# Kernel optimization log

Measured on AMD Instinct MI355X. Metric: run time of the kernel, lower is better.

The kernel has to match this reference:

```python
import jax, jax.numpy as jnp
import numpy as np

B, S, D, M, E, K = 2, 2048, 1024, 1408, 8, 2  # batch, seq, n_embed, n_moe_mlp, n_experts, top_k


def setup_inputs() -> dict:
    key = jax.random.key(0)
    k0, k1, k2, k3, k4 = jax.random.split(key, 5)
    scale = 0.02
    return {
        "x": jax.random.normal(k0, (B, S, D), dtype=jnp.float32),
        "w_gate": jax.random.normal(k1, (D, E), dtype=jnp.float32) * scale,  # gate.weight.T
        "w_g": jax.random.normal(k2, (E, D, M), dtype=jnp.float32) * scale,  # gate_proj.weight.T per expert
        "w_u": jax.random.normal(k3, (E, D, M), dtype=jnp.float32) * scale,  # up_proj.weight.T per expert
        "w_d": jax.random.normal(k4, (E, M, D), dtype=jnp.float32) * scale,  # down_proj.weight.T per expert
    }


def reference(x, w_gate, w_g, w_u, w_d):
    # router
    scores = x @ w_gate                                  # [B,S,E]
    topk_scores, topk_idx = jax.lax.top_k(scores, K)     # [B,S,K]
    topk_probs = jax.nn.softmax(topk_scores, axis=-1)    # softmax over selected experts only
    # scatter top-k probs back to dense [B,S,E] gating (top_k indices are distinct)
    gating = jnp.sum(
        jax.nn.one_hot(topk_idx, E, dtype=topk_probs.dtype) * topk_probs[..., None],
        axis=-2,
    )                                                    # [B,S,E]
    # dense all-expert SwiGLU (faithful to the compute-then-mask original)
    hidden = jax.nn.silu(jnp.einsum("bsd,edm->ebsm", x, w_g)) * jnp.einsum(
        "bsd,edm->ebsm", x, w_u
    )                                                    # [E,B,S,M]
    expert_out = jnp.einsum("ebsm,emd->ebsd", hidden, w_d)  # [E,B,S,D]
    # masked weighted combine
    y = jnp.einsum("bse,ebsd->bsd", gating, expert_out)  # [B,S,D]
    return y
```

## Files before the change

kernel.cpp:

```cpp
#include <hip/hip_runtime.h>
#include <cstdio>

constexpr int T  = 4096;
constexpr int D  = 1024;
constexpr int M  = 1408;
constexpr int E  = 8;

constexpr int TM = 128;
constexpr int TN = 128;
constexpr int BK = 32;
constexpr int MT_MAX = T / TM;
constexpr int NT_UP = M / TN;
constexpr int NT_DN = D / TN;
constexpr int RCAP = T * 2 + E * TM;

constexpr int CSTR = 64;
constexpr int XCV  = T / 2;
constexpr int TPW  = E * (D / 64) * (M / 64);
constexpr int PREP_GRID = XCV + 2 * TPW;
constexpr int NGEMM_UP  = E * MT_MAX * NT_UP;
constexpr int UPG_GRID  = NGEMM_UP + TPW;

typedef _Float16 half8 __attribute__((ext_vector_type(8)));
typedef float    floatx4 __attribute__((ext_vector_type(4)));

#define VMW12() asm volatile("s_waitcnt vmcnt(12)" ::: "memory")
#define VMW6()  asm volatile("s_waitcnt vmcnt(6)"  ::: "memory")
#define VMW4()  asm volatile("s_waitcnt vmcnt(4)"  ::: "memory")
#define VMW0()  asm volatile("s_waitcnt vmcnt(0)"  ::: "memory")

constexpr size_t OFF_COUNTS = 0;
constexpr size_t OFF_TLIST  = 2048;
constexpr size_t OFF_PLIST  = OFF_TLIST + (size_t)E * T * 4;
constexpr size_t OFF_XH     = OFF_PLIST + (size_t)E * T * 4;
constexpr size_t OFF_HID    = OFF_XH  + (size_t)T * D * 2;
constexpr size_t OFF_WGT    = OFF_HID + (size_t)RCAP * M * 2;
constexpr size_t OFF_WUT    = OFF_WGT + (size_t)E * M * D * 2;
constexpr size_t OFF_WDT    = OFF_WUT + (size_t)E * M * D * 2;
constexpr size_t WS_NEED    = OFF_WDT + (size_t)E * D * M * 2;

__device__ __forceinline__ void gl_lds16(const void* g, void* l) {
  __builtin_amdgcn_global_load_lds(
      (const __attribute__((address_space(1))) unsigned int*)g,
      (__attribute__((address_space(3))) unsigned int*)l, 16, 0, 0);
}

__device__ __forceinline__ void expert_base_pc(const int* __restrict__ counts,
                                               int e, int& base_e, int& pc_e,
                                               int& cnt_e) {
  int b = 0; base_e = 0; pc_e = 0; cnt_e = 0;
  #pragma unroll
  for (int ee = 0; ee < E; ++ee) {
    int c = counts[ee * CSTR];
    int p = (c + TM - 1) / TM * TM;
    if (ee == e) { base_e = b; pc_e = p; cnt_e = c; }
    b += p;
  }
}

__device__ __forceinline__ void transpose64(
    const float* __restrict__ src, _Float16* __restrict__ dst,
    int Rr, int Cc, int j, float (*tile)[69]) {
  int ctn = Cc >> 6, rtn = Rr >> 6;
  int e   = j / (ctn * rtn);
  int rem = j - e * (ctn * rtn);
  int rt = rem / ctn, ct = rem - rt * ctn;
  int t = threadIdx.x;
  int lr = t >> 2;
  int lc = (t & 3) * 16;
  const float* s = src + ((size_t)e * Rr + rt * 64 + lr) * Cc + ct * 64 + lc;
  float4 v0 = *(const float4*)(s + 0);
  float4 v1 = *(const float4*)(s + 4);
  float4 v2 = *(const float4*)(s + 8);
  float4 v3 = *(const float4*)(s + 12);
  float* tr = &tile[lr][lc];
  tr[0]  = v0.x; tr[1]  = v0.y; tr[2]  = v0.z; tr[3]  = v0.w;
  tr[4]  = v1.x; tr[5]  = v1.y; tr[6]  = v1.z; tr[7]  = v1.w;
  tr[8]  = v2.x; tr[9]  = v2.y; tr[10] = v2.z; tr[11] = v2.w;
  tr[12] = v3.x; tr[13] = v3.y; tr[14] = v3.z; tr[15] = v3.w;
  __syncthreads();
  #pragma unroll
  for (int rep = 0; rep < 2; ++rep) {
    int s2 = t + rep * 256;
    int oc = s2 >> 3;
    int sl = s2 & 7;
    half8 o;
    #pragma unroll
    for (int q = 0; q < 8; ++q) o[q] = (_Float16)tile[sl * 8 + q][oc];
    *(half8*)(dst + ((size_t)e * Cc + ct * 64 + oc) * Rr + rt * 64 + sl * 8) = o;
  }
}

__global__ __launch_bounds__(256) void k_prep(
    const float* __restrict__ x, const float* __restrict__ wgate,
    const float* __restrict__ w_g, const float* __restrict__ w_u,
    _Float16* __restrict__ Xh,
    _Float16* __restrict__ wgT, _Float16* __restrict__ wuT,
    int* __restrict__ counts, int* __restrict__ tlist,
    float* __restrict__ plist) {
  __shared__ float tile[64][69];
  __shared__ float s_red[4][8];
  int bid = blockIdx.x;

  if (bid < XCV) {
    int tid = threadIdx.x;
    int row  = tid >> 7;
    int t    = bid * 2 + row;
    int dpos = (tid & 127) * 8;
    int wv = tid >> 6, lane = tid & 63;
    const float* xr = x + (size_t)t * D + dpos;
    float4 v0 = *(const float4*)(xr);
    float4 v1 = *(const float4*)(xr + 4);
    half8 h;
    h[0] = (_Float16)v0.x; h[1] = (_Float16)v0.y;
    h[2] = (_Float16)v0.z; h[3] = (_Float16)v0.w;
    h[4] = (_Float16)v1.x; h[5] = (_Float16)v1.y;
    h[6] = (_Float16)v1.z; h[7] = (_Float16)v1.w;
    *(half8*)(Xh + (size_t)t * D + dpos) = h;
    float xv[8] = {v0.x, v0.y, v0.z, v0.w, v1.x, v1.y, v1.z, v1.w};
    float acc[8] = {0.f,0.f,0.f,0.f,0.f,0.f,0.f,0.f};
    #pragma unroll
    for (int j = 0; j < 8; ++j) {
      const float4* wr2 = (const float4*)(wgate + (size_t)(dpos + j) * E);
      float4 w0 = wr2[0], w1 = wr2[1];
      acc[0] += xv[j] * w0.x; acc[1] += xv[j] * w0.y;
      acc[2] += xv[j] * w0.z; acc[3] += xv[j] * w0.w;
      acc[4] += xv[j] * w1.x; acc[5] += xv[j] * w1.y;
      acc[6] += xv[j] * w1.z; acc[7] += xv[j] * w1.w;
    }
    #pragma unroll
    for (int e = 0; e < 8; ++e) {
      #pragma unroll
      for (int off = 32; off; off >>= 1) acc[e] += __shfl_xor(acc[e], off, 64);
    }
    if (lane == 0) {
      #pragma unroll
      for (int e = 0; e < 8; ++e) s_red[wv][e] = acc[e];
    }
    __syncthreads();
    if ((tid & 127) == 0) {
      int wb = row * 2;
      float sc[8];
      #pragma unroll
      for (int e = 0; e < 8; ++e) sc[e] = s_red[wb][e] + s_red[wb + 1][e];
      int i0 = 0; float s0 = sc[0];
      #pragma unroll
      for (int e = 1; e < 8; ++e) if (sc[e] > s0) { s0 = sc[e]; i0 = e; }
      int i1 = -1; float s1 = -1e30f;
      #pragma unroll
      for (int e = 0; e < 8; ++e) if (e != i0 && sc[e] > s1) { s1 = sc[e]; i1 = e; }
      float p0 = 1.f / (1.f + expf(s1 - s0));
      float p1 = 1.f - p0;
      int q0 = atomicAdd(&counts[i0 * CSTR], 1);
      int q1 = atomicAdd(&counts[i1 * CSTR], 1);
      tlist[i0 * T + q0] = t; plist[i0 * T + q0] = p0;
      tlist[i1 * T + q1] = t; plist[i1 * T + q1] = p1;
    }
    return;
  }

  int i = bid - XCV;
  if (i < TPW) transpose64(w_g, wgT, D, M, i, tile);
  else         transpose64(w_u, wuT, D, M, i - TPW, tile);
}

__global__ __launch_bounds__(256, 2) void k_upgate(
    const _Float16* __restrict__ Xh, const _Float16* __restrict__ wgT,
    const _Float16* __restrict__ wuT, _Float16* __restrict__ Hid,
    const int* __restrict__ counts, const int* __restrict__ tlist,
    const float* __restrict__ w_d, _Float16* __restrict__ wdT) {
  __shared__ _Float16 As[3][TM * BK];
  __shared__ _Float16 Bg[3][TN * BK];
  __shared__ _Float16 Bu[3][TN * BK];
  int lin = blockIdx.x;
  if (lin >= NGEMM_UP) {
    float (*tile)[69] = reinterpret_cast<float (*)[69]>(&As[0][0]);
    transpose64(w_d, wdT, M, D, lin - NGEMM_UP, tile);
    return;
  }
  int e = lin & 7;
  int r = lin >> 3;
  int nt = r % NT_UP;
  int mt = r / NT_UP;
  int base_e, pc_e, cnt_e;
  expert_base_pc(counts, e, base_e, pc_e, cnt_e);
  if (mt * TM >= pc_e) return;
  int row0 = base_e + mt * TM;
  int n0 = nt * TN;
  int tid = threadIdx.x;
  int w = tid >> 6, lane = tid & 63;
  int lrow = lane & 15, quad = lane >> 4;
  int wr = w >> 1, wc = w & 1;
  int sr = lane >> 2;
  int c4 = lane & 3;
  int swc = ((c4 ^ ((sr >> 1) & 3))) * 8;

  const _Float16* wg_e = wgT + (size_t)e * M * D;
  const _Float16* wu_e = wuT + (size_t)e * M * D;
  const _Float16* pA[2]; const _Float16* pG[2]; const _Float16* pU[2];
  int loff[2];
  #pragma unroll
  for (int is = 0; is < 2; ++is) {
    int grow = w * 32 + is * 16 + sr;
    int local = mt * TM + grow;
    int trow = (local < cnt_e) ? tlist[e * T + local] : 0;
    pA[is] = Xh   + (size_t)trow * D + swc;
    pG[is] = wg_e + (size_t)(n0 + grow) * D + swc;
    pU[is] = wu_e + (size_t)(n0 + grow) * D + swc;
    loff[is] = (w * 2 + is) * 1024;
  }

  int swr = (lrow >> 1) & 3;

  floatx4 accg[4][4] = {};
  floatx4 accu[4][4] = {};

  auto stage = [&](int b) {
    char* a0 = (char*)&As[b][0];
    char* g0 = (char*)&Bg[b][0];
    char* u0 = (char*)&Bu[b][0];
    #pragma unroll
    for (int is = 0; is < 2; ++is) {
      gl_lds16(pA[is], a0 + loff[is]); pA[is] += BK;
      gl_lds16(pG[is], g0 + loff[is]); pG[is] += BK;
      gl_lds16(pU[is], u0 + loff[is]); pU[is] += BK;
    }
  };
  auto compute = [&](int b) {
    int kc = (quad ^ swr) * 8;
    half8 af[4];
    #pragma unroll
    for (int i = 0; i < 4; ++i)
      af[i] = *(const half8*)&As[b][(wr * 64 + i * 16 + lrow) * BK + kc];
    #pragma unroll
    for (int c = 0; c < 4; ++c) {
      int bo = (wc * 64 + c * 16 + lrow) * BK + kc;
      half8 bgc = *(const half8*)&Bg[b][bo];
      half8 buc = *(const half8*)&Bu[b][bo];
      #pragma unroll
      for (int i = 0; i < 4; ++i) {
        accg[c][i] = __builtin_amdgcn_mfma_f32_16x16x32_f16(af[i], bgc, accg[c][i], 0, 0, 0);
        accu[c][i] = __builtin_amdgcn_mfma_f32_16x16x32_f16(af[i], buc, accu[c][i], 0, 0, 0);
      }
    }
  };

  constexpr int NTK = D / BK;
  stage(0); stage(1);
  for (int k = 0; k < NTK; ++k) {
    if (k + 2 < NTK) {
      stage((k + 2) % 3);
      VMW12();
    } else if (k + 1 < NTK) {
      VMW6();
    } else {
      VMW0();
    }
    __builtin_amdgcn_sched_barrier(0);
    __builtin_amdgcn_s_barrier();
    compute(k % 3);
    __builtin_amdgcn_s_barrier();
  }

  #pragma unroll
  for (int c = 0; c < 4; ++c) {
    int col = n0 + wc * 64 + c * 16 + lrow;
    #pragma unroll
    for (int i = 0; i < 4; ++i) {
      int rowb = row0 + wr * 64 + i * 16 + quad * 4;
      #pragma unroll
      for (int reg = 0; reg < 4; ++reg) {
        float g = accg[c][i][reg], u = accu[c][i][reg];
        Hid[(size_t)(rowb + reg) * M + col] = (_Float16)(g / (1.f + expf(-g)) * u);
      }
    }
  }
}

__global__ __launch_bounds__(256, 2) void k_down(
    const _Float16* __restrict__ Hid, const _Float16* __restrict__ wdT,
    float* __restrict__ out, const int* __restrict__ counts,
    const int* __restrict__ tlist, const float* __restrict__ plist) {
  int lin = blockIdx.x;
  int e = lin & 7;
  int r = lin >> 3;
  int nt = r % NT_DN;
  int mt = r / NT_DN;
  int base_e, pc_e, cnt_e;
  expert_base_pc(counts, e, base_e, pc_e, cnt_e);
  if (mt * TM >= pc_e) return;
  int row0 = base_e + mt * TM;
  int d0 = nt * TN;
  __shared__ _Float16 As[2][TM * BK];
  __shared__ _Float16 Bs[2][TN * BK];
  int tid = threadIdx.x;
  int w = tid >> 6, lane = tid & 63;
  int lrow = lane & 15, quad = lane >> 4;
  int wr = w >> 1, wc = w & 1;
  int sr = lane >> 2;
  int c4 = lane & 3;
  int swc = ((c4 ^ ((sr >> 1) & 3))) * 8;

  const _Float16* wd_e = wdT + (size_t)e * D * M;
  const _Float16* pA[2]; const _Float16* pB[2];
  int loff[2];
  #pragma unroll
  for (int is = 0; is < 2; ++is) {
    int grow = w * 32 + is * 16 + sr;
    pA[is] = Hid  + (size_t)(row0 + grow) * M + swc;
    pB[is] = wd_e + (size_t)(d0   + grow) * M + swc;
    loff[is] = (w * 2 + is) * 1024;
  }

  int swr = (lrow >> 1) & 3;

  floatx4 acc[4][4] = {};

  auto stage = [&](int b) {
    char* a0 = (char*)&As[b][0];
    char* b0 = (char*)&Bs[b][0];
    #pragma unroll
    for (int is = 0; is < 2; ++is) {
      gl_lds16(pA[is], a0 + loff[is]); pA[is] += BK;
      gl_lds16(pB[is], b0 + loff[is]); pB[is] += BK;
    }
  };
  auto compute = [&](int b) {
    int kc = (quad ^ swr) * 8;
    half8 af[4];
    #pragma unroll
    for (int i = 0; i < 4; ++i)
      af[i] = *(const half8*)&As[b][(wr * 64 + i * 16 + lrow) * BK + kc];
    #pragma unroll
    for (int c = 0; c < 4; ++c) {
      half8 bc = *(const half8*)&Bs[b][(wc * 64 + c * 16 + lrow) * BK + kc];
      #pragma unroll
      for (int i = 0; i < 4; ++i)
        acc[c][i] = __builtin_amdgcn_mfma_f32_16x16x32_f16(af[i], bc, acc[c][i], 0, 0, 0);
    }
  };

  constexpr int NTK = M / BK;
  stage(0);
  int cur = 0;
  for (int k = 0; k < NTK; ++k) {
    if (k + 1 < NTK) {
      stage(cur ^ 1);
      VMW4();
    } else {
      VMW0();
    }
    __builtin_amdgcn_sched_barrier(0);
    __builtin_amdgcn_s_barrier();
    compute(cur);
    __builtin_amdgcn_s_barrier();
    cur ^= 1;
  }

  int tI[4][4]; float pI[4][4];
  #pragma unroll
  for (int i = 0; i < 4; ++i) {
    #pragma unroll
    for (int reg = 0; reg < 4; ++reg) {
      int rl = mt * TM + wr * 64 + i * 16 + quad * 4 + reg;
      bool valid = rl < cnt_e;
      tI[i][reg] = valid ? tlist[e * T + rl] : -1;
      pI[i][reg] = valid ? plist[e * T + rl] : 0.f;
    }
  }
  #pragma unroll
  for (int c = 0; c < 4; ++c) {
    int col = d0 + wc * 64 + c * 16 + lrow;
    #pragma unroll
    for (int i = 0; i < 4; ++i) {
      #pragma unroll
      for (int reg = 0; reg < 4; ++reg) {
        if (tI[i][reg] >= 0)
          atomicAdd(&out[(size_t)tI[i][reg] * D + col], pI[i][reg] * acc[c][i][reg]);
      }
    }
  }
}

extern "C" void kernel_launch(void* const* d_in, const int* in_sizes, int n_in,
                              void* d_out, int out_size, void* d_ws, size_t ws_size,
                              hipStream_t stream) {
  const float* x     = (const float*)d_in[0];
  const float* wgate = (const float*)d_in[1];
  const float* w_g   = (const float*)d_in[2];
  const float* w_u   = (const float*)d_in[3];
  const float* w_d   = (const float*)d_in[4];
  float* out = (float*)d_out;
  char* ws = (char*)d_ws;

  if (ws_size < WS_NEED) {
    fprintf(stderr, "kernel_launch: ws_size=%zu < needed %zu\n", ws_size, WS_NEED);
    return;
  }

  int* counts   = (int*)(ws + OFF_COUNTS);
  int* tlist    = (int*)(ws + OFF_TLIST);
  float* plist  = (float*)(ws + OFF_PLIST);
  _Float16* Xh  = (_Float16*)(ws + OFF_XH);
  _Float16* Hid = (_Float16*)(ws + OFF_HID);
  _Float16* wgT = (_Float16*)(ws + OFF_WGT);
  _Float16* wuT = (_Float16*)(ws + OFF_WUT);
  _Float16* wdT = (_Float16*)(ws + OFF_WDT);

  hipMemsetAsync(counts, 0, (size_t)E * CSTR * 4, stream);
  hipMemsetAsync(out, 0, (size_t)T * D * 4, stream);

  k_prep<<<PREP_GRID, 256, 0, stream>>>(x, wgate, w_g, w_u, Xh,
                                        wgT, wuT, counts, tlist, plist);
  k_upgate<<<UPG_GRID, 256, 0, stream>>>(Xh, wgT, wuT, Hid, counts, tlist,
                                         w_d, wdT);
  k_down<<<E * MT_MAX * NT_DN, 256, 0, stream>>>(Hid, wdT, out, counts,
                                                 tlist, plist);
}
```

Measured before the change: 324.7 us.

## Replace atomic scatter in down GEMM with fp16 partials and gather combine kernel

The down-projection kernel now writes unweighted per-row fp16 results into a padded buffer that reuses the Xh region, instead of doing float atomicAdds into the output. A new combine kernel gathers each token's two expert rows and writes their weighted sum directly, which also removes the output memset. The down GEMM's k-loop moves from double to triple buffering. This adds an extra launch, a round trip through the partial buffer, and fp16 rounding of the per-expert outputs.

```diff
diff --git a/kernel.cpp b/kernel.cpp
--- a/kernel.cpp
+++ b/kernel.cpp
@@ -22,18 +22,22 @@
 constexpr int UPG_GRID  = NGEMM_UP + TPW;
 
 typedef _Float16 half8 __attribute__((ext_vector_type(8)));
+typedef _Float16 half4 __attribute__((ext_vector_type(4)));
 typedef float    floatx4 __attribute__((ext_vector_type(4)));
 
 #define VMW12() asm volatile("s_waitcnt vmcnt(12)" ::: "memory")
+#define VMW8()  asm volatile("s_waitcnt vmcnt(8)"  ::: "memory")
 #define VMW6()  asm volatile("s_waitcnt vmcnt(6)"  ::: "memory")
 #define VMW4()  asm volatile("s_waitcnt vmcnt(4)"  ::: "memory")
 #define VMW0()  asm volatile("s_waitcnt vmcnt(0)"  ::: "memory")
 
 constexpr size_t OFF_COUNTS = 0;
 constexpr size_t OFF_TLIST  = 2048;
-constexpr size_t OFF_PLIST  = OFF_TLIST + (size_t)E * T * 4;
-constexpr size_t OFF_XH     = OFF_PLIST + (size_t)E * T * 4;
-constexpr size_t OFF_HID    = OFF_XH  + (size_t)T * D * 2;
+constexpr size_t OFF_T2E    = OFF_TLIST + (size_t)E * T * 4;
+constexpr size_t OFF_T2POS  = OFF_T2E   + (size_t)2 * T * 4;
+constexpr size_t OFF_T2P    = OFF_T2POS + (size_t)2 * T * 4;
+constexpr size_t OFF_XG     = OFF_T2P   + (size_t)2 * T * 4;
+constexpr size_t OFF_HID    = OFF_XG  + (size_t)RCAP * D * 2;
 constexpr size_t OFF_WGT    = OFF_HID + (size_t)RCAP * M * 2;
 constexpr size_t OFF_WUT    = OFF_WGT + (size_t)E * M * D * 2;
 constexpr size_t OFF_WDT    = OFF_WUT + (size_t)E * M * D * 2;
@@ -97,7 +101,7 @@
     _Float16* __restrict__ Xh,
     _Float16* __restrict__ wgT, _Float16* __restrict__ wuT,
     int* __restrict__ counts, int* __restrict__ tlist,
-    float* __restrict__ plist) {
+    int* __restrict__ t2e, int* __restrict__ t2pos, float* __restrict__ t2p) {
   __shared__ float tile[64][69];
   __shared__ float s_red[4][8];
   int bid = blockIdx.x;
@@ -153,8 +157,10 @@
       float p1 = 1.f - p0;
       int q0 = atomicAdd(&counts[i0 * CSTR], 1);
       int q1 = atomicAdd(&counts[i1 * CSTR], 1);
-      tlist[i0 * T + q0] = t; plist[i0 * T + q0] = p0;
-      tlist[i1 * T + q1] = t; plist[i1 * T + q1] = p1;
+      tlist[i0 * T + q0] = t;
+      tlist[i1 * T + q1] = t;
+      t2e[2 * t]     = i0; t2pos[2 * t]     = q0; t2p[2 * t]     = p0;
+      t2e[2 * t + 1] = i1; t2pos[2 * t + 1] = q1; t2p[2 * t + 1] = p1;
     }
     return;
   }
@@ -279,8 +285,7 @@
 
 __global__ __launch_bounds__(256, 2) void k_down(
     const _Float16* __restrict__ Hid, const _Float16* __restrict__ wdT,
-    float* __restrict__ out, const int* __restrict__ counts,
-    const int* __restrict__ tlist, const float* __restrict__ plist) {
+    _Float16* __restrict__ Yp, const int* __restrict__ counts) {
   int lin = blockIdx.x;
   int e = lin & 7;
   int r = lin >> 3;
@@ -291,8 +296,8 @@
   if (mt * TM >= pc_e) return;
   int row0 = base_e + mt * TM;
   int d0 = nt * TN;
-  __shared__ _Float16 As[2][TM * BK];
-  __shared__ _Float16 Bs[2][TN * BK];
+  __shared__ _Float16 As[3][TM * BK];
+  __shared__ _Float16 Bs[3][TN * BK];
   int tid = threadIdx.x;
   int w = tid >> 6, lane = tid & 63;
   int lrow = lane & 15, quad = lane >> 4;
@@ -341,45 +346,61 @@
   };
 
   constexpr int NTK = M / BK;
-  stage(0);
-  int cur = 0;
+  stage(0); stage(1);
   for (int k = 0; k < NTK; ++k) {
-    if (k + 1 < NTK) {
-      stage(cur ^ 1);
+    if (k + 2 < NTK) {
+      stage((k + 2) % 3);
+      VMW8();
+    } else if (k + 1 < NTK) {
       VMW4();
     } else {
       VMW0();
     }
     __builtin_amdgcn_sched_barrier(0);
     __builtin_amdgcn_s_barrier();
-    compute(cur);
+    compute(k % 3);
     __builtin_amdgcn_s_barrier();
-    cur ^= 1;
-  }
-
-  int tI[4][4]; float pI[4][4];
-  #pragma unroll
-  for (int i = 0; i < 4; ++i) {
-    #pragma unroll
-    for (int reg = 0; reg < 4; ++reg) {
-      int rl = mt * TM + wr * 64 + i * 16 + quad * 4 + reg;
-      bool valid = rl < cnt_e;
-      tI[i][reg] = valid ? tlist[e * T + rl] : -1;
-      pI[i][reg] = valid ? plist[e * T + rl] : 0.f;
-    }
-  }
+  }
+
   #pragma unroll
   for (int c = 0; c < 4; ++c) {
     int col = d0 + wc * 64 + c * 16 + lrow;
     #pragma unroll
     for (int i = 0; i < 4; ++i) {
-      #pragma unroll
-      for (int reg = 0; reg < 4; ++reg) {
-        if (tI[i][reg] >= 0)
-          atomicAdd(&out[(size_t)tI[i][reg] * D + col], pI[i][reg] * acc[c][i][reg]);
-      }
-    }
-  }
+      int rowb = row0 + wr * 64 + i * 16 + quad * 4;
+      #pragma unroll
+      for (int reg = 0; reg < 4; ++reg)
+        Yp[(size_t)(rowb + reg) * D + col] = (_Float16)acc[c][i][reg];
+    }
+  }
+}
+
+__global__ __launch_bounds__(256) void k_combine(
+    const _Float16* __restrict__ Yp, const int* __restrict__ counts,
+    const int* __restrict__ t2e, const int* __restrict__ t2pos,
+    const float* __restrict__ t2p, float* __restrict__ out) {
+  int t = blockIdx.x;
+  int e0 = t2e[2 * t], e1 = t2e[2 * t + 1];
+  int b = 0, b0 = 0, b1 = 0;
+  #pragma unroll
+  for (int ee = 0; ee < E; ++ee) {
+    if (ee == e0) b0 = b;
+    if (ee == e1) b1 = b;
+    int c = counts[ee * CSTR];
+    b += (c + TM - 1) / TM * TM;
+  }
+  int r0 = b0 + t2pos[2 * t];
+  int r1 = b1 + t2pos[2 * t + 1];
+  float p0 = t2p[2 * t], p1 = t2p[2 * t + 1];
+  int d = threadIdx.x * 4;
+  half4 h0 = *(const half4*)(Yp + (size_t)r0 * D + d);
+  half4 h1 = *(const half4*)(Yp + (size_t)r1 * D + d);
+  float4 o;
+  o.x = p0 * (float)h0.x + p1 * (float)h1.x;
+  o.y = p0 * (float)h0.y + p1 * (float)h1.y;
+  o.z = p0 * (float)h0.z + p1 * (float)h1.z;
+  o.w = p0 * (float)h0.w + p1 * (float)h1.w;
+  *(float4*)(out + (size_t)t * D + d) = o;
 }
 
 extern "C" void kernel_launch(void* const* d_in, const int* in_sizes, int n_in,
@@ -400,20 +421,23 @@
 
   int* counts   = (int*)(ws + OFF_COUNTS);
   int* tlist    = (int*)(ws + OFF_TLIST);
-  float* plist  = (float*)(ws + OFF_PLIST);
-  _Float16* Xh  = (_Float16*)(ws + OFF_XH);
+  int* t2e      = (int*)(ws + OFF_T2E);
+  int* t2pos    = (int*)(ws + OFF_T2POS);
+  float* t2p    = (float*)(ws + OFF_T2P);
+  _Float16* Xh  = (_Float16*)(ws + OFF_XG);
   _Float16* Hid = (_Float16*)(ws + OFF_HID);
   _Float16* wgT = (_Float16*)(ws + OFF_WGT);
   _Float16* wuT = (_Float16*)(ws + OFF_WUT);
   _Float16* wdT = (_Float16*)(ws + OFF_WDT);
 
   hipMemsetAsync(counts, 0, (size_t)E * CSTR * 4, stream);
-  hipMemsetAsync(out, 0, (size_t)T * D * 4, stream);
 
   k_prep<<<PREP_GRID, 256, 0, stream>>>(x, wgate, w_g, w_u, Xh,
-                                        wgT, wuT, counts, tlist, plist);
+                                        wgT, wuT, counts, tlist,
+                                        t2e, t2pos, t2p);
   k_upgate<<<UPG_GRID, 256, 0, stream>>>(Xh, wgT, wuT, Hid, counts, tlist,
                                          w_d, wdT);
-  k_down<<<E * MT_MAX * NT_DN, 256, 0, stream>>>(Hid, wdT, out, counts,
-                                                 tlist, plist);
-}
+  _Float16* Yp = Xh;
+  k_down<<<E * MT_MAX * NT_DN, 256, 0, stream>>>(Hid, wdT, Yp, counts);
+  k_combine<<<T, 256, 0, stream>>>(Yp, counts, t2e, t2pos, t2p, out);
+}
```

After: 299.8 us. 1.08x faster.
